# Optimization experiments

Hardware: AMD Instinct MI355X
Metric: run time of the kernel (lower is better)

Reference implementation:

```python
import jax, jax.numpy as jnp
import numpy as np

B, T, N, H = 512, 128, 128, 256


def setup_inputs() -> dict:
    key = jax.random.key(0)
    ks = jax.random.split(key, 8)
    rn = lambda k, shape, sc: (jax.random.normal(k, shape, jnp.float32) * sc)
    return {
        "data": rn(ks[0], (B, T, N), 1.0),
        "h0": jnp.zeros((B, H), jnp.float32),
        # SimpleRNNCell params: h_t = tanh(x@Wx + h@Wh + b)
        "Wx": rn(ks[1], (N, H), 0.05),
        "Wh": rn(ks[2], (H, H), 0.05),
        "b": jnp.zeros((H,), jnp.float32),
        # InputAttention: w1: Dense(T) over last dim T; w2: Dense(T) over hidden; v: Dense(1)
        "W1": rn(ks[3], (T, T), 0.05),
        "b1": jnp.zeros((T,), jnp.float32),
        "W2": rn(ks[4], (H, T), 0.05),
        "b2": jnp.zeros((T,), jnp.float32),
        "Wv": rn(ks[5], (T, 1), 0.05),
        "bv": jnp.zeros((1,), jnp.float32),
        "n": N,
    }


def reference(data, h0, Wx, Wh, b, W1, b1, W2, b2, Wv, bv, n):
    # data: (B, T, n); h0: (B, H)
    Tlen = data.shape[1]
    x_perm = jnp.swapaxes(data, 1, 2)          # (B, n, T) == Permute((2,1))(x)
    pre = x_perm @ W1 + b1                      # w1(x_perm): loop-invariant, hoisted

    def step(h, x_t):
        # SimpleRNNCell: new state used for this step's attention
        h_new = jnp.tanh(x_t @ Wx + h @ Wh + b)                 # (B, H)
        q = h_new @ W2 + b2                                      # w2(RepeatVector(n)(h)) per row -> (B, T)
        score = jnp.tanh(pre + q[:, None, :])                    # (B, n, T)
        e = score @ Wv + bv                                      # (B, n, 1)
        e = jnp.swapaxes(e, 1, 2)                                # Permute((2,1)) -> (B, 1, n)
        alpha = jax.nn.softmax(e, axis=-1)                       # softmax over n
        return h_new, alpha

    xs = jnp.swapaxes(data, 0, 1)               # (T, B, n): data[:, t, :] per step
    _, alphas = jax.lax.scan(step, h0, xs)      # (T, B, 1, n)
    # faithful to tf.reshape(alpha_seq.stack(), (-1, T, n))
    alpha_seq = alphas.reshape(-1, Tlen, n)     # (B, T, n)
    return data * alpha_seq
```

## Files before the change

kernel.cpp:

```cpp
#include <hip/hip_runtime.h>


#define C2L 2.8853900817779268f
#define L2E 1.4426950408889634f

typedef _Float16 hf;
typedef _Float16 hf2 __attribute__((ext_vector_type(2)));
typedef _Float16 hf4 __attribute__((ext_vector_type(4)));
typedef _Float16 hf8 __attribute__((ext_vector_type(8)));
typedef float f32x4 __attribute__((ext_vector_type(4)));

__device__ __forceinline__ float fast_exp2(float x){
#if __has_builtin(__builtin_amdgcn_exp2f)
  return __builtin_amdgcn_exp2f(x);
#else
  return exp2f(x);
#endif
}
__device__ __forceinline__ float fast_rcp(float x){
#if __has_builtin(__builtin_amdgcn_rcpf)
  return __builtin_amdgcn_rcpf(x);
#else
  return 1.f/x;
#endif
}

__global__ __launch_bounds__(256) void k_prep_w(const float* __restrict__ Wx,
    const float* __restrict__ W2, const float* __restrict__ W1,
    hf* __restrict__ wts){
  int tid = blockIdx.x*256 + threadIdx.x;
  if (tid < 32768){
    int n = tid >> 7, k = tid & 127;
    wts[tid] = (hf)Wx[k*256 + n];
  } else if (tid < 65536){
    int t2 = tid - 32768;
    int n = t2 >> 8, k = t2 & 255;
    wts[tid] = (hf)W2[k*128 + n];
  } else {
    int t3 = tid - 65536;
    int n = t3 >> 7, k = t3 & 127;
    wts[tid] = (hf)W1[k*128 + n];
  }
}

template<int K, int MODE>
__global__ __launch_bounds__(256) void k_gemm(const void* __restrict__ Asrc,
    const hf* __restrict__ Bt, const float* __restrict__ bias,
    float* __restrict__ Cout){
  constexpr int SA = 136;
  __shared__ alignas(16) hf As[64*SA];
  __shared__ alignas(16) hf Bs[128*SA];
  const int tid = threadIdx.x;
  const int w = tid >> 6, lane = tid & 63;
  const int c = lane & 15, q = lane >> 4;
  const int bx = blockIdx.x;
  const int col0 = (MODE==0) ? blockIdx.y*128 : 0;

  float br[8];
  #pragma unroll
  for (int ni=0; ni<8; ni++) br[ni] = bias[col0 + ni*16 + c];

  f32x4 acc[8];
  #pragma unroll
  for (int ni=0; ni<8; ni++) acc[ni] = (f32x4){0.f,0.f,0.f,0.f};

  for (int kc=0; kc<K/128; kc++){
    if (MODE == 0){
      const float* A = (const float*)Asrc + (long)bx*64*128;
      #pragma unroll
      for (int v=0; v<8; v++){
        int f4 = v*256 + tid;
        int m = f4 >> 5, k4 = (f4 & 31)*4;
        float4 d = *(const float4*)&A[m*128 + k4];
        hf4 h = {(hf)d.x,(hf)d.y,(hf)d.z,(hf)d.w};
        *(hf4*)&As[m*SA + k4] = h;
      }
    } else if (MODE == 1){
      const hf* A = (const hf*)Asrc + (long)bx*64*256;
      #pragma unroll
      for (int v=0; v<4; v++){
        int f8 = v*256 + tid;
        int m = f8 >> 4, k8 = (f8 & 15)*8;
        *(hf8*)&As[m*SA + k8] = *(const hf8*)&A[m*256 + kc*128 + k8];
      }
    } else {
      const float* A = (const float*)Asrc + (long)(bx>>1)*16384;
      const int i0 = (bx & 1)*64;
      #pragma unroll
      for (int v=0; v<8; v++){
        int f4 = v*256 + tid;
        int t = f4 >> 4, i4 = (f4 & 15)*4;
        float4 d = *(const float4*)&A[t*128 + i0 + i4];
        As[(i4+0)*SA + t] = (hf)d.x;
        As[(i4+1)*SA + t] = (hf)d.y;
        As[(i4+2)*SA + t] = (hf)d.z;
        As[(i4+3)*SA + t] = (hf)d.w;
      }
    }
    #pragma unroll
    for (int v=0; v<8; v++){
      int f8 = v*256 + tid;
      int n = f8 >> 4, k8 = (f8 & 15)*8;
      *(hf8*)&Bs[n*SA + k8] = *(const hf8*)&Bt[(col0+n)*K + kc*128 + k8];
    }
    __syncthreads();
    #pragma unroll
    for (int kk=0; kk<4; kk++){
      hf8 a = *(const hf8*)&As[(w*16 + c)*SA + kk*32 + q*8];
      #pragma unroll
      for (int ni=0; ni<8; ni++){
        hf8 b = *(const hf8*)&Bs[(ni*16 + c)*SA + kk*32 + q*8];
        acc[ni] = __builtin_amdgcn_mfma_f32_16x16x32_f16(a, b, acc[ni], 0, 0, 0);
      }
    }
    __syncthreads();
  }
  #pragma unroll
  for (int ni=0; ni<8; ni++){
    #pragma unroll
    for (int r=0; r<4; r++){
      int rloc = w*16 + q*4 + r;
      int col = col0 + ni*16 + c;
      float val = acc[ni][r] + br[ni];
      int addr;
      if (MODE == 0){
        int R = bx*64 + rloc;
        int b_ = R >> 7, t_ = R & 127;
        addr = (t_*512 + b_)*256 + col;
      } else if (MODE == 1){
        int R = bx*64 + rloc;
        addr = R*128 + col;
        val = fast_exp2(C2L*val);
      } else {
        int b_ = bx >> 1, i_ = (bx & 1)*64 + rloc;
        addr = b_*16384 + i_*128 + col;
        val = fast_exp2(C2L*val);
      }
      Cout[addr] = val;
    }
  }
}

__global__ __launch_bounds__(1024, 4) void k_rnn(const float* __restrict__ h0,
    const float* __restrict__ Wh, const float* __restrict__ xw,
    hf* __restrict__ Hb){
  __shared__ alignas(16) char hs[2*8192];
  const int tid = threadIdx.x;
  const int w = tid >> 6, lane = tid & 63;
  const int c = lane & 15, q = lane >> 4;
  const int b0 = blockIdx.x * 16;
  const int col = w*16 + c;
  hf8 bw[8];
  #pragma unroll
  for (int kc=0; kc<8; kc++){
    #pragma unroll
    for (int e=0; e<8; e++){
      bw[kc][e] = (hf)Wh[(kc*32 + q*8 + e)*256 + col];
    }
  }
  if (tid < 512){
    int m = tid >> 5, s8 = tid & 31;
    const float* src = &h0[(b0 + m)*256 + s8*8];
    float4 d0 = *(const float4*)&src[0];
    float4 d1 = *(const float4*)&src[4];
    hf8 hv = {(hf)d0.x,(hf)d0.y,(hf)d0.z,(hf)d0.w,
              (hf)d1.x,(hf)d1.y,(hf)d1.z,(hf)d1.w};
    *(hf8*)&hs[m*512 + ((s8 ^ (m & 7)) << 4)] = hv;
  }
  float xwv[4];
  #pragma unroll
  for (int r=0; r<4; r++) xwv[r] = xw[(b0 + q*4 + r)*256 + col];
  __syncthreads();
  const int m = c;
  const int abase = m*512;
  for (int t=0; t<128; t++){
    const int p = t & 1;
    float xwn[4];
    if (t < 127){
      #pragma unroll
      for (int r=0; r<4; r++) xwn[r] = xw[((t+1)*512 + b0 + q*4 + r)*256 + col];
    } else {
      #pragma unroll
      for (int r=0; r<4; r++) xwn[r] = 0.f;
    }
    hf8 a[8];
    #pragma unroll
    for (int kc=0; kc<8; kc++)
      a[kc] = *(const hf8*)&hs[p*8192 + abase + ((((kc<<2)|q) ^ (m & 7)) << 4)];
    f32x4 acca = (f32x4){0.f,0.f,0.f,0.f};
    f32x4 accb = (f32x4){0.f,0.f,0.f,0.f};
    #pragma unroll
    for (int kc=0; kc<4; kc++){
      acca = __builtin_amdgcn_mfma_f32_16x16x32_f16(a[kc],   bw[kc],   acca, 0,0,0);
      accb = __builtin_amdgcn_mfma_f32_16x16x32_f16(a[kc+4], bw[kc+4], accb, 0,0,0);
    }
    #pragma unroll
    for (int r=0; r<4; r++){
      float v = acca[r] + accb[r] + xwv[r];
      float e2 = fast_exp2(v*C2L);
      float hn = 1.f - 2.f*fast_rcp(e2 + 1.f);
      int row = q*4 + r;
      *(hf*)&hs[(p^1)*8192 + row*512
                + (((col >> 3) ^ (row & 7)) << 4) + (col & 7)*2] = (hf)hn;
      Hb[(t*512 + b0 + row)*256 + col] = (hf)hn;
      xwv[r] = xwn[r];
    }
    __syncthreads();
  }
}

__global__ __launch_bounds__(512, 4) void k_attn(const float* __restrict__ P,
    const float* __restrict__ Qm, const float* __restrict__ Wv,
    const float* __restrict__ data, float* __restrict__ out){
  __shared__ alignas(16) float qs[32*128];
  __shared__ alignas(16) float wvs[128];
  __shared__ alignas(16) float epart[2][4][4][128];
  __shared__ float red[2][4][2];
  const int b = blockIdx.x, tile = blockIdx.y;
  const int tid = threadIdx.x;
  const int i = tid & 127, g = tid >> 7;
  const int t0 = tile*32;
  if (tid < 128) wvs[tid] = -2.f*Wv[tid];
  #pragma unroll
  for (int v=0; v<2; v++){
    int flat = v*2048 + tid*4;
    int tt = flat >> 7, c = flat & 127;
    *(float4*)&qs[flat] = *(const float4*)&Qm[((t0+tt)*512 + b)*128 + c];
  }
  float4 p4[8];
  const float* prow = P + b*16384 + i*128 + g*32;
  #pragma unroll
  for (int v=0; v<8; v++) p4[v] = *(const float4*)&prow[v*4];
  __syncthreads();
  for (int tp=0; tp<8; tp++){
    const int pp = tp & 1;
    const float* qb  = &qs[(4*tp)*128 + g*32];
    const float* wvr = &wvs[g*32];
    float acc0=0.f, acc1=0.f, acc2=0.f, acc3=0.f;
    #pragma unroll
    for (int mm=0; mm<8; mm++){
      float4 Pv = p4[mm];
      float4 wv = *(const float4*)&wvr[mm*4];
      #pragma unroll
      for (int tl=0; tl<4; tl++){
        float4 qq = *(const float4*)&qb[tl*128 + mm*4];
        float u = fmaf(Pv.x, qq.x, 1.f), v = fmaf(Pv.y, qq.y, 1.f);
        float x = fmaf(Pv.z, qq.z, 1.f), y = fmaf(Pv.w, qq.w, 1.f);
        float d01 = u*v, d23 = x*y;
        float n01 = fmaf(wv.x, v, wv.y*u);
        float n23 = fmaf(wv.z, y, wv.w*x);
        float N = fmaf(n01, d23, n23*d01);
        float r = fast_rcp(d01*d23);
        float term = N*r;
        if (tl==0) acc0 += term;
        else if (tl==1) acc1 += term;
        else if (tl==2) acc2 += term;
        else acc3 += term;
      }
    }
    epart[pp][g][0][i] = acc0;
    epart[pp][g][1][i] = acc1;
    epart[pp][g][2][i] = acc2;
    epart[pp][g][3][i] = acc3;
    __syncthreads();
    float e = epart[pp][0][g][i] + epart[pp][1][g][i]
            + epart[pp][2][g][i] + epart[pp][3][g][i];
    float pe = fast_exp2(e*L2E);
    float sm = pe;
    #pragma unroll
    for (int off=32; off; off>>=1) sm += __shfl_xor(sm, off);
    if ((tid & 63) == 0) red[pp][g][(tid>>6)&1] = sm;
    __syncthreads();
    float ssum = red[pp][g][0] + red[pp][g][1];
    float alpha = pe * fast_rcp(ssum);
    int t = t0 + 4*tp + g;
    int base = (t*512 + b)*128 + i;
    out[base] = data[base]*alpha;
  }
}

extern "C" void kernel_launch(void* const* d_in, const int* in_sizes, int n_in,
                              void* d_out, int out_size, void* d_ws, size_t ws_size,
                              hipStream_t stream) {
  const float* data = (const float*)d_in[0];
  const float* h0   = (const float*)d_in[1];
  const float* Wx   = (const float*)d_in[2];
  const float* Wh   = (const float*)d_in[3];
  const float* bb   = (const float*)d_in[4];
  const float* W1   = (const float*)d_in[5];
  const float* b1   = (const float*)d_in[6];
  const float* W2   = (const float*)d_in[7];
  const float* b2   = (const float*)d_in[8];
  const float* Wv   = (const float*)d_in[9];
  float* wsp = (float*)d_ws;
  float* P   = wsp;
  float* xwQ = wsp + 8388608;
  hf*    Hbf = (hf*)(wsp + 25165824);
  hf*    wts = (hf*)(wsp + 33554432);
  const hf* Wxt = wts;
  const hf* W2t = wts + 32768;
  const hf* W1t = wts + 65536;
  float* out = (float*)d_out;

  hipLaunchKernelGGL(k_prep_w, dim3(320), dim3(256), 0, stream, Wx, W2, W1, wts);
  hipLaunchKernelGGL((k_gemm<128,0>), dim3(1024,2), dim3(256), 0, stream,
                     (const void*)data, Wxt, bb, xwQ);
  hipLaunchKernelGGL((k_gemm<128,2>), dim3(1024),   dim3(256), 0, stream,
                     (const void*)data, W1t, b1, P);
  hipLaunchKernelGGL(k_rnn, dim3(32), dim3(1024), 0, stream, h0, Wh, xwQ, Hbf);
  hipLaunchKernelGGL((k_gemm<256,1>), dim3(1024),   dim3(256), 0, stream,
                     (const void*)Hbf, W2t, b2, xwQ);
  hipLaunchKernelGGL(k_attn, dim3(512, 4), dim3(512), 0, stream, P, xwQ, Wv, data, out);
}
```

Measured before the change: 354.2 us.

## Halve RNN block size, give each wave two column tiles, prefetch xw two steps ahead

```diff
diff --git a/kernel.cpp b/kernel.cpp
--- a/kernel.cpp
+++ b/kernel.cpp
@@ -5,7 +5,6 @@
 #define L2E 1.4426950408889634f
 
 typedef _Float16 hf;
-typedef _Float16 hf2 __attribute__((ext_vector_type(2)));
 typedef _Float16 hf4 __attribute__((ext_vector_type(4)));
 typedef _Float16 hf8 __attribute__((ext_vector_type(8)));
 typedef float f32x4 __attribute__((ext_vector_type(4)));
@@ -141,7 +140,7 @@
   }
 }
 
-__global__ __launch_bounds__(1024, 4) void k_rnn(const float* __restrict__ h0,
+__global__ __launch_bounds__(512, 2) void k_rnn(const float* __restrict__ h0,
     const float* __restrict__ Wh, const float* __restrict__ xw,
     hf* __restrict__ Hb){
   __shared__ alignas(16) char hs[2*8192];
@@ -149,16 +148,19 @@
   const int w = tid >> 6, lane = tid & 63;
   const int c = lane & 15, q = lane >> 4;
   const int b0 = blockIdx.x * 16;
-  const int col = w*16 + c;
-  hf8 bw[8];
-  #pragma unroll
-  for (int kc=0; kc<8; kc++){
-    #pragma unroll
-    for (int e=0; e<8; e++){
-      bw[kc][e] = (hf)Wh[(kc*32 + q*8 + e)*256 + col];
-    }
-  }
-  if (tid < 512){
+  const int w0 = w * 32;
+  hf8 bw[2][8];
+  #pragma unroll
+  for (int nt=0; nt<2; nt++){
+    #pragma unroll
+    for (int kc=0; kc<8; kc++){
+      #pragma unroll
+      for (int e=0; e<8; e++){
+        bw[nt][kc][e] = (hf)Wh[(kc*32 + q*8 + e)*256 + w0 + nt*16 + c];
+      }
+    }
+  }
+  {
     int m = tid >> 5, s8 = tid & 31;
     const float* src = &h0[(b0 + m)*256 + s8*8];
     float4 d0 = *(const float4*)&src[0];
@@ -167,45 +169,73 @@
               (hf)d1.x,(hf)d1.y,(hf)d1.z,(hf)d1.w};
     *(hf8*)&hs[m*512 + ((s8 ^ (m & 7)) << 4)] = hv;
   }
-  float xwv[4];
-  #pragma unroll
-  for (int r=0; r<4; r++) xwv[r] = xw[(b0 + q*4 + r)*256 + col];
+  float bufA[2][4], bufB[2][4];
+  #pragma unroll
+  for (int nt=0; nt<2; nt++){
+    #pragma unroll
+    for (int r=0; r<4; r++){
+      bufA[nt][r] = xw[(0*512 + b0 + q*4 + r)*256 + w0 + nt*16 + c];
+      bufB[nt][r] = xw[(1*512 + b0 + q*4 + r)*256 + w0 + nt*16 + c];
+    }
+  }
   __syncthreads();
-  const int m = c;
-  const int abase = m*512;
-  for (int t=0; t<128; t++){
-    const int p = t & 1;
-    float xwn[4];
-    if (t < 127){
-      #pragma unroll
-      for (int r=0; r<4; r++) xwn[r] = xw[((t+1)*512 + b0 + q*4 + r)*256 + col];
-    } else {
-      #pragma unroll
-      for (int r=0; r<4; r++) xwn[r] = 0.f;
-    }
-    hf8 a[8];
-    #pragma unroll
-    for (int kc=0; kc<8; kc++)
-      a[kc] = *(const hf8*)&hs[p*8192 + abase + ((((kc<<2)|q) ^ (m & 7)) << 4)];
-    f32x4 acca = (f32x4){0.f,0.f,0.f,0.f};
-    f32x4 accb = (f32x4){0.f,0.f,0.f,0.f};
-    #pragma unroll
-    for (int kc=0; kc<4; kc++){
-      acca = __builtin_amdgcn_mfma_f32_16x16x32_f16(a[kc],   bw[kc],   acca, 0,0,0);
-      accb = __builtin_amdgcn_mfma_f32_16x16x32_f16(a[kc+4], bw[kc+4], accb, 0,0,0);
-    }
-    #pragma unroll
-    for (int r=0; r<4; r++){
-      float v = acca[r] + accb[r] + xwv[r];
-      float e2 = fast_exp2(v*C2L);
-      float hn = 1.f - 2.f*fast_rcp(e2 + 1.f);
-      int row = q*4 + r;
-      *(hf*)&hs[(p^1)*8192 + row*512
-                + (((col >> 3) ^ (row & 7)) << 4) + (col & 7)*2] = (hf)hn;
-      Hb[(t*512 + b0 + row)*256 + col] = (hf)hn;
-      xwv[r] = xwn[r];
-    }
-    __syncthreads();
+  const int abase = c*512;
+  #pragma unroll 1
+  for (int t=0; t<128; t+=2){
+    #pragma unroll
+    for (int half=0; half<2; half++){
+      const int T = t + half;
+      const int p = T & 1;
+      hf8 a[8];
+      #pragma unroll
+      for (int kc=0; kc<8; kc++)
+        a[kc] = *(const hf8*)&hs[p*8192 + abase + ((((kc<<2)|q) ^ (c & 7)) << 4)];
+      f32x4 ac0a = (f32x4){0.f,0.f,0.f,0.f}, ac0b = ac0a;
+      f32x4 ac1a = ac0a, ac1b = ac0a;
+      #pragma unroll
+      for (int kc=0; kc<4; kc++){
+        ac0a = __builtin_amdgcn_mfma_f32_16x16x32_f16(a[kc],   bw[0][kc],   ac0a,0,0,0);
+        ac1a = __builtin_amdgcn_mfma_f32_16x16x32_f16(a[kc],   bw[1][kc],   ac1a,0,0,0);
+        ac0b = __builtin_amdgcn_mfma_f32_16x16x32_f16(a[kc+4], bw[0][kc+4], ac0b,0,0,0);
+        ac1b = __builtin_amdgcn_mfma_f32_16x16x32_f16(a[kc+4], bw[1][kc+4], ac1b,0,0,0);
+      }
+      float vv[2][4];
+      #pragma unroll
+      for (int r=0; r<4; r++){
+        vv[0][r] = ac0a[r] + ac0b[r] + (half ? bufB[0][r] : bufA[0][r]);
+        vv[1][r] = ac1a[r] + ac1b[r] + (half ? bufB[1][r] : bufA[1][r]);
+      }
+      #pragma unroll
+      for (int nt=0; nt<2; nt++){
+        #pragma unroll
+        for (int r=0; r<4; r++){
+          float nv = (T+2 < 128)
+            ? xw[((T+2)*512 + b0 + q*4 + r)*256 + w0 + nt*16 + c] : 0.f;
+          if (half) bufB[nt][r] = nv; else bufA[nt][r] = nv;
+        }
+      }
+      #pragma unroll
+      for (int nt=0; nt<2; nt++){
+        #pragma unroll
+        for (int pr=0; pr<2; pr++){
+          float ea = fast_exp2(vv[nt][2*pr+0]*C2L) + 1.f;
+          float eb = fast_exp2(vv[nt][2*pr+1]*C2L) + 1.f;
+          float R = fast_rcp(ea*eb);
+          float h0v = fmaf(-2.f*eb, R, 1.f);
+          float h1v = fmaf(-2.f*ea, R, 1.f);
+          #pragma unroll
+          for (int rr=0; rr<2; rr++){
+            float hn = rr ? h1v : h0v;
+            int row = q*4 + 2*pr + rr;
+            int col = w0 + nt*16 + c;
+            *(hf*)&hs[(p^1)*8192 + row*512
+                      + (((col >> 3) ^ (row & 7)) << 4) + (col & 7)*2] = (hf)hn;
+            Hb[(T*512 + b0 + row)*256 + col] = (hf)hn;
+          }
+        }
+      }
+      __syncthreads();
+    }
   }
 }
 
@@ -307,7 +337,7 @@
                      (const void*)data, Wxt, bb, xwQ);
   hipLaunchKernelGGL((k_gemm<128,2>), dim3(1024),   dim3(256), 0, stream,
                      (const void*)data, W1t, b1, P);
-  hipLaunchKernelGGL(k_rnn, dim3(32), dim3(1024), 0, stream, h0, Wh, xwQ, Hbf);
+  hipLaunchKernelGGL(k_rnn, dim3(32), dim3(512), 0, stream, h0, Wh, xwQ, Hbf);
   hipLaunchKernelGGL((k_gemm<256,1>), dim3(1024),   dim3(256), 0, stream,
                      (const void*)Hbf, W2t, b2, xwQ);
   hipLaunchKernelGGL(k_attn, dim3(512, 4), dim3(512), 0, stream, P, xwQ, Wv, data, out);
```

Result: slower. 372.8 us (+5.2%).
